# Optimization experiments

Measured on AMD Instinct MI355X. Metric: run time of the kernel, lower is better.

The kernel has to match this reference:

```python
import jax, jax.numpy as jnp
import numpy as np

N, T, S = 8192, 512, 4
ND, NC = 8, 16


def setup_inputs() -> dict:
    key = jax.random.key(0)
    ks = jax.random.split(key, 8)
    return {
        "drivers": jax.random.normal(ks[0], (N, T, ND), jnp.float32),
        "covariates": jax.random.normal(ks[1], (N, T, NC), jnp.float32),
        "Y": jax.random.normal(ks[2], (N, T, 1), jnp.float32),
        "eps": jax.random.normal(ks[3], (S, N, T, 1), jnp.float32),
        "tilde_psi": jnp.array([0.5], jnp.float32),
        "gamma_w": jax.random.normal(ks[4], (1, ND), jnp.float32) * 0.1,
        "alpha_w": jax.random.normal(ks[5], (1, NC), jnp.float32) * 0.1,
        "alpha_Y_lag": jnp.array([0.1], jnp.float32),
        "log_tilde_sigma": jnp.array([-1.0], jnp.float32),
        "mu_init": jnp.array([0.0], jnp.float32),
        "log_sigma_init": jnp.array([0.0], jnp.float32),
    }


def reference(drivers, covariates, Y, eps, tilde_psi, gamma_w, alpha_w,
              alpha_Y_lag, log_tilde_sigma, mu_init, log_sigma_init):
    psi = tilde_psi[0]
    sigma = jnp.exp(log_tilde_sigma[0])
    sigma0 = jnp.exp(log_sigma_init[0])

    # Structural drift gamma^T D_t + alpha^T W_t for all t in parallel: (N, T)
    proj = (jnp.einsum('ntd,d->nt', drivers, gamma_w[0])
            + jnp.einsum('ntc,c->nt', covariates, alpha_w[0]))
    # b_t for t>=1 includes lagged-outcome term alpha_Y_lag * Y_{t-1}: (N, T-1)
    b = proj[:, 1:] + alpha_Y_lag[0] * Y[:, :-1, 0]

    # Initial step (use_Y_in_init=False): mu_0 = mu_init + proj_0
    mu0 = mu_init[0] + proj[:, 0]                      # (N,)
    e = eps[..., 0]                                    # (S, N, T)
    Z0 = mu0[None, :] + sigma0 * e[:, :, 0]            # (S, N)

    def step(Z, xs):
        b_t, e_t = xs                                  # (N,), (S, N)
        mu_t = psi * Z + b_t[None, :]
        Z_new = mu_t + sigma * e_t
        return Z_new, (Z_new, mu_t)

    xs = (b.T, jnp.moveaxis(e[:, :, 1:], 2, 0))        # (T-1, N), (T-1, S, N)
    _, (Zs, mus) = jax.lax.scan(step, Z0, xs)          # each (T-1, S, N)

    Z_all = jnp.concatenate([Z0[None], Zs], axis=0)    # (T, S, N)
    mu_all = jnp.concatenate([jnp.broadcast_to(mu0, (S, N))[None], mus], axis=0)

    Z_out = jnp.moveaxis(Z_all, 0, 2)[..., None]       # (S, N, T, 1)
    mu_out = jnp.moveaxis(mu_all, 0, 2)[..., None]

    lv0 = jnp.broadcast_to(2.0 * log_sigma_init[0], (S, N, 1))
    lvt = jnp.broadcast_to(2.0 * log_tilde_sigma[0], (S, N, T - 1))
    lv_out = jnp.concatenate([lv0, lvt], axis=2)[..., None]

    return Z_out, mu_out, lv_out
```

## Files before the change

### kernel.cpp

```cpp
#include <hip/hip_runtime.h>

#define N 8192
#define T 512
#define S 4

__device__ __forceinline__ float dot4(float4 a, float4 b) {
    return a.x*b.x + a.y*b.y + a.z*b.z + a.w*b.w;
}
__device__ __forceinline__ int swz(int c) { return c ^ ((c >> 3) & 7); }

__global__ __launch_bounds__(256) void k_fused(
        const float* __restrict__ drivers,
        const float* __restrict__ cov,
        const float* __restrict__ Y,
        const float* __restrict__ eps,
        const float* __restrict__ tilde_psi,
        const float* __restrict__ gamma_w,
        const float* __restrict__ alpha_w,
        const float* __restrict__ alpha_Y_lag,
        const float* __restrict__ log_tilde_sigma,
        const float* __restrict__ mu_init,
        const float* __restrict__ log_sigma_init,
        float* __restrict__ Zout,
        float* __restrict__ muout,
        float* __restrict__ lvout) {
    __shared__ float4 dstage[512];
    __shared__ float4 cstage[1024];
    __shared__ float4 b_s4[128];
    float* b_s = (float*)b_s4;

    const int tid  = threadIdx.x;
    const int lane = tid & 63;
    const int w    = tid >> 6;
    const int n    = blockIdx.x;

    const float psi    = tilde_psi[0];
    const float lts    = log_tilde_sigma[0];
    const float lsi    = log_sigma_init[0];
    const float sigma  = expf(lts);
    const float sigma0 = expf(lsi);
    const float aY     = alpha_Y_lag[0];
    const float mu0c   = mu_init[0];

    const float4* g4 = (const float4*)gamma_w;
    const float4* a4 = (const float4*)alpha_w;
    const float4 g0 = g4[0], g1 = g4[1];
    const float4 w0 = a4[0], w1 = a4[1], w2 = a4[2], w3 = a4[3];

    const size_t chain = ((size_t)w * N + n) * (T / 4);
    const float4* e4 = (const float4*)eps + chain;
    const float4 eA = e4[lane];
    const float4 eB = e4[64 + lane];

    const float4* drv4 = (const float4*)drivers + (size_t)n * (T * 2);
    const float4* cov4 = (const float4*)cov     + (size_t)n * (T * 4);
    const float*  Yrow = Y + (size_t)n * T;

    #pragma unroll
    for (int h = 0; h < 2; ++h) {
        if (h) __syncthreads();
        dstage[swz(tid)]       = drv4[h * 512 + tid];
        dstage[swz(tid + 256)] = drv4[h * 512 + 256 + tid];
        #pragma unroll
        for (int k = 0; k < 4; ++k)
            cstage[swz(tid + 256 * k)] = cov4[h * 1024 + tid + 256 * k];
        const int t = h * 256 + tid;
        const float yprev = (t > 0) ? Yrow[t - 1] : 0.f;
        __syncthreads();
        const float4 dA = dstage[swz(2 * tid)];
        const float4 dB = dstage[swz(2 * tid + 1)];
        const float4 cA = cstage[swz(4 * tid)];
        const float4 cB = cstage[swz(4 * tid + 1)];
        const float4 cC = cstage[swz(4 * tid + 2)];
        const float4 cD = cstage[swz(4 * tid + 3)];
        const float proj = dot4(dA, g0) + dot4(dB, g1)
                         + dot4(cA, w0) + dot4(cB, w1)
                         + dot4(cC, w2) + dot4(cD, w3);
        b_s[t] = (t == 0) ? (mu0c + proj) : (proj + aY * yprev);
    }
    __syncthreads();

    const float pj1 = psi, pj2 = psi * psi, pj3 = pj2 * psi, pj4 = pj2 * pj2;
    const float wd0 = pj4, wd1 = wd0 * wd0, wd2 = wd1 * wd1,
                wd3 = wd2 * wd2, wd4 = wd3 * wd3, wd5 = wd4 * wd4;
    float p4l = 1.f;
    {
        float pw = pj4;
        p4l *= (lane & 1)  ? pw : 1.f; pw *= pw;
        p4l *= (lane & 2)  ? pw : 1.f; pw *= pw;
        p4l *= (lane & 4)  ? pw : 1.f; pw *= pw;
        p4l *= (lane & 8)  ? pw : 1.f; pw *= pw;
        p4l *= (lane & 16) ? pw : 1.f; pw *= pw;
        p4l *= (lane & 32) ? pw : 1.f;
    }

    float4* z4 = (float4*)Zout  + chain;
    float4* m4 = (float4*)muout + chain;
    float4* l4 = (float4*)lvout + chain;
    const float lvv = 2.f * lts;

    float Zlast = 0.f;
    #pragma unroll
    for (int seg = 0; seg < 2; ++seg) {
        const float4 e  = seg ? eB : eA;
        const float4 bq = b_s4[seg * 64 + lane];

        const float sg0 = (seg == 0 && lane == 0) ? sigma0 : sigma;
        const float z0 = bq.x + sg0 * e.x;
        const float z1 = psi * z0 + (bq.y + sigma * e.y);
        const float z2 = psi * z1 + (bq.z + sigma * e.z);
        const float z3 = psi * z2 + (bq.w + sigma * e.w);

        float v = z3, up;
        up = __shfl_up(v, 1);  v += (lane >= 1)  ? wd0 * up : 0.f;
        up = __shfl_up(v, 2);  v += (lane >= 2)  ? wd1 * up : 0.f;
        up = __shfl_up(v, 4);  v += (lane >= 4)  ? wd2 * up : 0.f;
        up = __shfl_up(v, 8);  v += (lane >= 8)  ? wd3 * up : 0.f;
        up = __shfl_up(v, 16); v += (lane >= 16) ? wd4 * up : 0.f;
        up = __shfl_up(v, 32); v += (lane >= 32) ? wd5 * up : 0.f;

        float Zprev = __shfl_up(v, 1);
        Zprev = (lane == 0) ? 0.f : Zprev;
        Zprev += p4l * Zlast;

        const float Z0 = z0 + pj1 * Zprev;
        const float Z1 = z1 + pj2 * Zprev;
        const float Z2 = z2 + pj3 * Zprev;
        const float Z3 = z3 + pj4 * Zprev;

        const float mu0 = Z0 - sg0   * e.x;
        const float mu1 = Z1 - sigma * e.y;
        const float mu2 = Z2 - sigma * e.z;
        const float mu3 = Z3 - sigma * e.w;

        z4[seg * 64 + lane] = make_float4(Z0, Z1, Z2, Z3);
        m4[seg * 64 + lane] = make_float4(mu0, mu1, mu2, mu3);
        l4[seg * 64 + lane] = (seg == 0 && lane == 0)
                            ? make_float4(2.f * lsi, lvv, lvv, lvv)
                            : make_float4(lvv, lvv, lvv, lvv);

        Zlast = __shfl(Z3, 63);
    }
}

extern "C" void kernel_launch(void* const* d_in, const int* in_sizes, int n_in,
                              void* d_out, int out_size, void* d_ws, size_t ws_size,
                              hipStream_t stream) {
    const float* drivers   = (const float*)d_in[0];
    const float* cov       = (const float*)d_in[1];
    const float* Y         = (const float*)d_in[2];
    const float* eps       = (const float*)d_in[3];
    const float* tilde_psi = (const float*)d_in[4];
    const float* gamma_w   = (const float*)d_in[5];
    const float* alpha_w   = (const float*)d_in[6];
    const float* aY        = (const float*)d_in[7];
    const float* lts       = (const float*)d_in[8];
    const float* mu_init   = (const float*)d_in[9];
    const float* lsi       = (const float*)d_in[10];

    float* out   = (float*)d_out;
    const size_t SNT = (size_t)S * N * T;
    float* Zout  = out;
    float* muout = out + SNT;
    float* lvout = out + 2 * SNT;

    k_fused<<<N, 256, 0, stream>>>(drivers, cov, Y, eps, tilde_psi,
                                   gamma_w, alpha_w, aY, lts, mu_init, lsi,
                                   Zout, muout, lvout);
}
```

Before: 140.9 us.

## Load drivers/covariates straight to registers and reduce projections with lane shuffles

Replaces the swizzled LDS staging of driver and covariate rows with direct coalesced float4 loads into registers. Each lane computes a partial dot product against the matching weight slice, and xor-shuffles combine the partials into per-timestep projections written to a small shared buffer. All global loads are issued up front, before the eps loads, and launch bounds now request 6 blocks per CU. The intent is to cut LDS traffic and barriers and raise occupancy, at the cost of more live registers and a Y load per lane inside the reduction loop.

```diff
diff --git a/kernel.cpp b/kernel.cpp
--- a/kernel.cpp
+++ b/kernel.cpp
@@ -7,9 +7,8 @@
 __device__ __forceinline__ float dot4(float4 a, float4 b) {
     return a.x*b.x + a.y*b.y + a.z*b.z + a.w*b.w;
 }
-__device__ __forceinline__ int swz(int c) { return c ^ ((c >> 3) & 7); }
 
-__global__ __launch_bounds__(256) void k_fused(
+__global__ __launch_bounds__(256, 6) void k_fused(
         const float* __restrict__ drivers,
         const float* __restrict__ cov,
         const float* __restrict__ Y,
@@ -24,10 +23,7 @@
         float* __restrict__ Zout,
         float* __restrict__ muout,
         float* __restrict__ lvout) {
-    __shared__ float4 dstage[512];
-    __shared__ float4 cstage[1024];
-    __shared__ float4 b_s4[128];
-    float* b_s = (float*)b_s4;
+    __shared__ __align__(16) float b_s[T];
 
     const int tid  = threadIdx.x;
     const int lane = tid & 63;
@@ -46,37 +42,42 @@
     const float4* a4 = (const float4*)alpha_w;
     const float4 g0 = g4[0], g1 = g4[1];
     const float4 w0 = a4[0], w1 = a4[1], w2 = a4[2], w3 = a4[3];
+    const float4 myg = (tid & 1) ? g1 : g0;
+    const float4 myw = (tid & 1) ? ((tid & 2) ? w3 : w1)
+                                 : ((tid & 2) ? w2 : w0);
+
+    const float4* drv4 = (const float4*)drivers + (size_t)n * (T * 2);
+    const float4* cov4 = (const float4*)cov     + (size_t)n * (T * 4);
+    const float*  Yrow = Y + (size_t)n * T;
+
+    float4 dL[4], cL[8];
+    #pragma unroll
+    for (int p = 0; p < 4; ++p) dL[p] = drv4[p * 256 + tid];
+    #pragma unroll
+    for (int q = 0; q < 8; ++q) cL[q] = cov4[q * 256 + tid];
 
     const size_t chain = ((size_t)w * N + n) * (T / 4);
     const float4* e4 = (const float4*)eps + chain;
     const float4 eA = e4[lane];
     const float4 eB = e4[64 + lane];
 
-    const float4* drv4 = (const float4*)drivers + (size_t)n * (T * 2);
-    const float4* cov4 = (const float4*)cov     + (size_t)n * (T * 4);
-    const float*  Yrow = Y + (size_t)n * T;
+    #pragma unroll
+    for (int p = 0; p < 4; ++p) {
+        float pd = dot4(dL[p], myg);
+        pd += __shfl_xor(pd, 1);
+        if ((lane & 1) == 0) b_s[(p * 256 + tid) >> 1] = pd;
+    }
+    __syncthreads();
 
     #pragma unroll
-    for (int h = 0; h < 2; ++h) {
-        if (h) __syncthreads();
-        dstage[swz(tid)]       = drv4[h * 512 + tid];
-        dstage[swz(tid + 256)] = drv4[h * 512 + 256 + tid];
-        #pragma unroll
-        for (int k = 0; k < 4; ++k)
-            cstage[swz(tid + 256 * k)] = cov4[h * 1024 + tid + 256 * k];
-        const int t = h * 256 + tid;
-        const float yprev = (t > 0) ? Yrow[t - 1] : 0.f;
-        __syncthreads();
-        const float4 dA = dstage[swz(2 * tid)];
-        const float4 dB = dstage[swz(2 * tid + 1)];
-        const float4 cA = cstage[swz(4 * tid)];
-        const float4 cB = cstage[swz(4 * tid + 1)];
-        const float4 cC = cstage[swz(4 * tid + 2)];
-        const float4 cD = cstage[swz(4 * tid + 3)];
-        const float proj = dot4(dA, g0) + dot4(dB, g1)
-                         + dot4(cA, w0) + dot4(cB, w1)
-                         + dot4(cC, w2) + dot4(cD, w3);
-        b_s[t] = (t == 0) ? (mu0c + proj) : (proj + aY * yprev);
+    for (int q = 0; q < 8; ++q) {
+        const int t = (q * 256 + tid) >> 2;
+        const float yv = (t > 0) ? Yrow[t - 1] : 0.f;
+        float pc = dot4(cL[q], myw);
+        pc += __shfl_xor(pc, 1);
+        pc += __shfl_xor(pc, 2);
+        if ((lane & 3) == 0)
+            b_s[t] += pc + ((t == 0) ? mu0c : aY * yv);
     }
     __syncthreads();
 
@@ -94,6 +95,7 @@
         p4l *= (lane & 32) ? pw : 1.f;
     }
 
+    const float4* b_s4 = (const float4*)b_s;
     float4* z4 = (float4*)Zout  + chain;
     float4* m4 = (float4*)muout + chain;
     float4* l4 = (float4*)lvout + chain;
```

After: 156.4 us. 11.0% more time.

## Split fused kernel into bias-projection and scan kernels via workspace buffer

Applied to the files above, without the earlier changes.

Splits the single fused kernel into two. k_bias computes the drift bias b for all (n,t) with direct vectorized global loads, replacing the swizzled LDS staging. k_scan reads b from a workspace and runs the warp-level parallel scan, handling 4 series per block. When the workspace is too small, b is written into the lv output buffer and a third kernel rewrites lv afterwards. This removes LDS staging and syncs, at the cost of an extra global round-trip for b and an additional launch.

```diff
diff --git a/kernel.cpp b/kernel.cpp
--- a/kernel.cpp
+++ b/kernel.cpp
@@ -7,78 +7,60 @@
 __device__ __forceinline__ float dot4(float4 a, float4 b) {
     return a.x*b.x + a.y*b.y + a.z*b.z + a.w*b.w;
 }
-__device__ __forceinline__ int swz(int c) { return c ^ ((c >> 3) & 7); }
 
-__global__ __launch_bounds__(256) void k_fused(
+__global__ __launch_bounds__(256) void k_bias(
         const float* __restrict__ drivers,
         const float* __restrict__ cov,
         const float* __restrict__ Y,
-        const float* __restrict__ eps,
-        const float* __restrict__ tilde_psi,
         const float* __restrict__ gamma_w,
         const float* __restrict__ alpha_w,
         const float* __restrict__ alpha_Y_lag,
+        const float* __restrict__ mu_init,
+        float* __restrict__ b) {
+    const float4* g4 = (const float4*)gamma_w;
+    const float4* a4 = (const float4*)alpha_w;
+    const float4 g0 = g4[0], g1 = g4[1];
+    const float4 w0 = a4[0], w1 = a4[1], w2 = a4[2], w3 = a4[3];
+    const float aY   = alpha_Y_lag[0];
+    const float mu0c = mu_init[0];
+
+    const size_t base = (size_t)blockIdx.x * 2048 + threadIdx.x;
+    const float4* d4 = (const float4*)drivers;
+    const float4* c4 = (const float4*)cov;
+
+    #pragma unroll 2
+    for (int it = 0; it < 8; ++it) {
+        const size_t id = base + (size_t)it * 256;
+        float4 dA = d4[id * 2], dB = d4[id * 2 + 1];
+        float4 cA = c4[id * 4], cB = c4[id * 4 + 1];
+        float4 cC = c4[id * 4 + 2], cD = c4[id * 4 + 3];
+        const float yprev = Y[id > 0 ? id - 1 : 0];
+        const float proj = dot4(dA, g0) + dot4(dB, g1)
+                         + dot4(cA, w0) + dot4(cB, w1)
+                         + dot4(cC, w2) + dot4(cD, w3);
+        const int t = (int)(id & (T - 1));
+        b[id] = (t == 0) ? (mu0c + proj) : (proj + aY * yprev);
+    }
+}
+
+__global__ __launch_bounds__(256) void k_scan(
+        const float* __restrict__ bg,
+        const float* __restrict__ eps,
+        const float* __restrict__ tilde_psi,
         const float* __restrict__ log_tilde_sigma,
-        const float* __restrict__ mu_init,
         const float* __restrict__ log_sigma_init,
         float* __restrict__ Zout,
         float* __restrict__ muout,
         float* __restrict__ lvout) {
-    __shared__ float4 dstage[512];
-    __shared__ float4 cstage[1024];
-    __shared__ float4 b_s4[128];
-    float* b_s = (float*)b_s4;
-
-    const int tid  = threadIdx.x;
-    const int lane = tid & 63;
-    const int w    = tid >> 6;
-    const int n    = blockIdx.x;
+    const int lane = threadIdx.x & 63;
+    const int w    = threadIdx.x >> 6;
 
     const float psi    = tilde_psi[0];
     const float lts    = log_tilde_sigma[0];
     const float lsi    = log_sigma_init[0];
     const float sigma  = expf(lts);
     const float sigma0 = expf(lsi);
-    const float aY     = alpha_Y_lag[0];
-    const float mu0c   = mu_init[0];
-
-    const float4* g4 = (const float4*)gamma_w;
-    const float4* a4 = (const float4*)alpha_w;
-    const float4 g0 = g4[0], g1 = g4[1];
-    const float4 w0 = a4[0], w1 = a4[1], w2 = a4[2], w3 = a4[3];
-
-    const size_t chain = ((size_t)w * N + n) * (T / 4);
-    const float4* e4 = (const float4*)eps + chain;
-    const float4 eA = e4[lane];
-    const float4 eB = e4[64 + lane];
-
-    const float4* drv4 = (const float4*)drivers + (size_t)n * (T * 2);
-    const float4* cov4 = (const float4*)cov     + (size_t)n * (T * 4);
-    const float*  Yrow = Y + (size_t)n * T;
-
-    #pragma unroll
-    for (int h = 0; h < 2; ++h) {
-        if (h) __syncthreads();
-        dstage[swz(tid)]       = drv4[h * 512 + tid];
-        dstage[swz(tid + 256)] = drv4[h * 512 + 256 + tid];
-        #pragma unroll
-        for (int k = 0; k < 4; ++k)
-            cstage[swz(tid + 256 * k)] = cov4[h * 1024 + tid + 256 * k];
-        const int t = h * 256 + tid;
-        const float yprev = (t > 0) ? Yrow[t - 1] : 0.f;
-        __syncthreads();
-        const float4 dA = dstage[swz(2 * tid)];
-        const float4 dB = dstage[swz(2 * tid + 1)];
-        const float4 cA = cstage[swz(4 * tid)];
-        const float4 cB = cstage[swz(4 * tid + 1)];
-        const float4 cC = cstage[swz(4 * tid + 2)];
-        const float4 cD = cstage[swz(4 * tid + 3)];
-        const float proj = dot4(dA, g0) + dot4(dB, g1)
-                         + dot4(cA, w0) + dot4(cB, w1)
-                         + dot4(cC, w2) + dot4(cD, w3);
-        b_s[t] = (t == 0) ? (mu0c + proj) : (proj + aY * yprev);
-    }
-    __syncthreads();
+    const float lvv    = 2.f * lts;
 
     const float pj1 = psi, pj2 = psi * psi, pj3 = pj2 * psi, pj4 = pj2 * pj2;
     const float wd0 = pj4, wd1 = wd0 * wd0, wd2 = wd1 * wd1,
@@ -94,53 +76,69 @@
         p4l *= (lane & 32) ? pw : 1.f;
     }
 
-    float4* z4 = (float4*)Zout  + chain;
-    float4* m4 = (float4*)muout + chain;
-    float4* l4 = (float4*)lvout + chain;
-    const float lvv = 2.f * lts;
+    #pragma unroll 1
+    for (int it = 0; it < 4; ++it) {
+        const int n = blockIdx.x * 4 + it;
+        const size_t chain = ((size_t)w * N + n) * (T / 4);
+        const float4* e4  = (const float4*)eps + chain;
+        const float4* b4  = (const float4*)bg + (size_t)n * (T / 4);
+        const float4 eA = e4[lane],      eB = e4[64 + lane];
+        const float4 bA = b4[lane],      bB = b4[64 + lane];
 
-    float Zlast = 0.f;
-    #pragma unroll
-    for (int seg = 0; seg < 2; ++seg) {
-        const float4 e  = seg ? eB : eA;
-        const float4 bq = b_s4[seg * 64 + lane];
+        float4* z4 = (float4*)Zout  + chain;
+        float4* m4 = (float4*)muout + chain;
+        float4* l4 = (float4*)lvout + chain;
 
-        const float sg0 = (seg == 0 && lane == 0) ? sigma0 : sigma;
-        const float z0 = bq.x + sg0 * e.x;
-        const float z1 = psi * z0 + (bq.y + sigma * e.y);
-        const float z2 = psi * z1 + (bq.z + sigma * e.z);
-        const float z3 = psi * z2 + (bq.w + sigma * e.w);
+        float Zlast = 0.f;
+        #pragma unroll
+        for (int seg = 0; seg < 2; ++seg) {
+            const float4 e  = seg ? eB : eA;
+            const float4 bq = seg ? bB : bA;
 
-        float v = z3, up;
-        up = __shfl_up(v, 1);  v += (lane >= 1)  ? wd0 * up : 0.f;
-        up = __shfl_up(v, 2);  v += (lane >= 2)  ? wd1 * up : 0.f;
-        up = __shfl_up(v, 4);  v += (lane >= 4)  ? wd2 * up : 0.f;
-        up = __shfl_up(v, 8);  v += (lane >= 8)  ? wd3 * up : 0.f;
-        up = __shfl_up(v, 16); v += (lane >= 16) ? wd4 * up : 0.f;
-        up = __shfl_up(v, 32); v += (lane >= 32) ? wd5 * up : 0.f;
+            const float sg0 = (seg == 0 && lane == 0) ? sigma0 : sigma;
+            const float z0 = bq.x + sg0 * e.x;
+            const float z1 = psi * z0 + (bq.y + sigma * e.y);
+            const float z2 = psi * z1 + (bq.z + sigma * e.z);
+            const float z3 = psi * z2 + (bq.w + sigma * e.w);
 
-        float Zprev = __shfl_up(v, 1);
-        Zprev = (lane == 0) ? 0.f : Zprev;
-        Zprev += p4l * Zlast;
+            float v = z3, up;
+            up = __shfl_up(v, 1);  v += (lane >= 1)  ? wd0 * up : 0.f;
+            up = __shfl_up(v, 2);  v += (lane >= 2)  ? wd1 * up : 0.f;
+            up = __shfl_up(v, 4);  v += (lane >= 4)  ? wd2 * up : 0.f;
+            up = __shfl_up(v, 8);  v += (lane >= 8)  ? wd3 * up : 0.f;
+            up = __shfl_up(v, 16); v += (lane >= 16) ? wd4 * up : 0.f;
+            up = __shfl_up(v, 32); v += (lane >= 32) ? wd5 * up : 0.f;
 
-        const float Z0 = z0 + pj1 * Zprev;
-        const float Z1 = z1 + pj2 * Zprev;
-        const float Z2 = z2 + pj3 * Zprev;
-        const float Z3 = z3 + pj4 * Zprev;
+            float Zprev = __shfl_up(v, 1);
+            Zprev = (lane == 0) ? 0.f : Zprev;
+            Zprev += p4l * Zlast;
 
-        const float mu0 = Z0 - sg0   * e.x;
-        const float mu1 = Z1 - sigma * e.y;
-        const float mu2 = Z2 - sigma * e.z;
-        const float mu3 = Z3 - sigma * e.w;
+            const float Z0 = z0 + pj1 * Zprev;
+            const float Z1 = z1 + pj2 * Zprev;
+            const float Z2 = z2 + pj3 * Zprev;
+            const float Z3 = z3 + pj4 * Zprev;
 
-        z4[seg * 64 + lane] = make_float4(Z0, Z1, Z2, Z3);
-        m4[seg * 64 + lane] = make_float4(mu0, mu1, mu2, mu3);
-        l4[seg * 64 + lane] = (seg == 0 && lane == 0)
-                            ? make_float4(2.f * lsi, lvv, lvv, lvv)
-                            : make_float4(lvv, lvv, lvv, lvv);
+            z4[seg * 64 + lane] = make_float4(Z0, Z1, Z2, Z3);
+            m4[seg * 64 + lane] = make_float4(Z0 - sg0 * e.x, Z1 - sigma * e.y,
+                                              Z2 - sigma * e.z, Z3 - sigma * e.w);
+            l4[seg * 64 + lane] = (seg == 0 && lane == 0)
+                                ? make_float4(2.f * lsi, lvv, lvv, lvv)
+                                : make_float4(lvv, lvv, lvv, lvv);
 
-        Zlast = __shfl(Z3, 63);
+            Zlast = __shfl(Z3, 63);
+        }
     }
+}
+
+__global__ __launch_bounds__(256) void k_lv(
+        float* __restrict__ lv,
+        const float* __restrict__ lts,
+        const float* __restrict__ lsi) {
+    int i = blockIdx.x * blockDim.x + threadIdx.x;
+    float v = 2.0f * lts[0];
+    float4 o = make_float4(v, v, v, v);
+    if ((i & (T / 4 - 1)) == 0) o.x = 2.0f * lsi[0];
+    ((float4*)lv)[i] = o;
 }
 
 extern "C" void kernel_launch(void* const* d_in, const int* in_sizes, int n_in,
@@ -164,7 +162,15 @@
     float* muout = out + SNT;
     float* lvout = out + 2 * SNT;
 
-    k_fused<<<N, 256, 0, stream>>>(drivers, cov, Y, eps, tilde_psi,
-                                   gamma_w, alpha_w, aY, lts, mu_init, lsi,
-                                   Zout, muout, lvout);
+    const size_t bbytes = (size_t)N * T * sizeof(float);
+    const bool ws_ok = (ws_size >= bbytes);
+    float* b = ws_ok ? (float*)d_ws : lvout;
+
+    k_bias<<<(N * T) / 2048, 256, 0, stream>>>(drivers, cov, Y, gamma_w,
+                                               alpha_w, aY, mu_init, b);
+    k_scan<<<N / 4, 256, 0, stream>>>(b, eps, tilde_psi, lts, lsi,
+                                      Zout, muout, lvout);
+    if (!ws_ok) {
+        k_lv<<<(SNT / 4) / 256, 256, 0, stream>>>(lvout, lts, lsi);
+    }
 }
```

Result: slower. 173.0 us (+22.8%).
